# Kernel optimization log

Measured on AMD Instinct MI355X. Metric: run time of the kernel, lower is better.

The kernel has to match this reference:

```python
import jax, jax.numpy as jnp
import numpy as np

LOG2 = 0.6931471805599453

def ssp(x):
    # shifted softplus: softplus(x) - log(2)
    return jax.nn.softplus(x) - LOG2

def residual(v, W, b):
    # PhysNetResidual reuses the same linear twice: linear(act(linear(act(x)))) + x
    h = ssp(v) @ W + b
    h = ssp(h) @ W + b
    return h + v

def setup_inputs() -> dict:
    key = jax.random.key(0)
    ks = jax.random.split(key, 20)
    N, E, D, R = 50000, 600000, 128, 32
    n_int, n_atom_res, n_out_res = 3, 1, 1
    def orth(k, shape):
        return jax.random.orthogonal(k, shape[0])[: shape[0], : shape[1]].astype(jnp.float32) if shape[0] == shape[1] else jax.random.normal(k, shape, jnp.float32) * (1.0 / np.sqrt(shape[0]))
    return {
        "x": jax.random.normal(ks[0], (N, D), jnp.float32),
        "g_ij": jax.random.uniform(ks[1], (E, R), jnp.float32),
        "Wf": orth(ks[2], (D, D)), "bf": jnp.zeros((D,), jnp.float32),
        "Wg": jax.random.normal(ks[3], (R, D), jnp.float32) * (1.0 / np.sqrt(R)),
        "Wj": orth(ks[4], (D, D)), "bj": jnp.zeros((D,), jnp.float32),
        "Wi": orth(ks[5], (D, D)), "bi": jnp.zeros((D,), jnp.float32),
        "u": jnp.ones((D,), jnp.float32),
        "rWint": jnp.stack([orth(ks[6 + i], (D, D)) for i in range(n_int)]),
        "rbint": jnp.zeros((n_int, D), jnp.float32),
        "rWatom": jnp.stack([orth(ks[10 + i], (D, D)) for i in range(n_atom_res)]),
        "rbatom": jnp.zeros((n_atom_res, D), jnp.float32),
        "rWout": jnp.stack([orth(ks[12 + i], (D, D)) for i in range(n_out_res)]),
        "rbout": jnp.zeros((n_out_res, D), jnp.float32),
        "idx_i": jax.random.randint(ks[14], (E,), 0, N, jnp.int32),
        "idx_j": jax.random.randint(ks[15], (E,), 0, N, jnp.int32),
        "n_atoms": N,
    }

def reference(x, g_ij, Wf, bf, Wg, Wj, bj, Wi, bi, u,
              rWint, rbint, rWatom, rbatom, rWout, rbout,
              idx_i, idx_j, n_atoms):
    # --- PhysNetInteraction ---
    xa = ssp(x)                                   # [N, D]
    x_j = xa[idx_j]                               # gather -> [E, D]
    xp = u * xa                                   # [N, D]
    vp = ssp(x_j @ Wj + bj) * (g_ij @ Wg)         # [E, D] RBF-gated messages
    vm = ssp(xa @ Wi + bi)                        # [N, D]
    v = jax.ops.segment_sum(vp, idx_i, num_segments=n_atoms) + vm
    for k in range(rWint.shape[0]):
        v = residual(v, rWint[k], rbint[k])
    v = ssp(v)
    h = xp + v @ Wf + bf                          # [N, D]
    # --- atomic residual stack ---
    for k in range(rWatom.shape[0]):
        h = residual(h, rWatom[k], rbatom[k])
    # --- PhysNetOutput ---
    o = h
    for k in range(rWout.shape[0]):
        o = residual(o, rWout[k], rbout[k])
    o = ssp(o)
    return (o, h)
```

## Files before the change

### kernel.cpp

```cpp
#include <hip/hip_runtime.h>
#include <stdint.h>

#define LOG2F 0.693147180559945f

typedef __attribute__((ext_vector_type(8))) short short8;
typedef __attribute__((ext_vector_type(4))) float f32x4;

__device__ __forceinline__ float ssp(float x){
  float t = __expf(-fabsf(x));
  return fmaxf(x, 0.0f) + __logf(1.0f + t) - LOG2F;
}

__device__ __forceinline__ uint32_t bf16rn(float x){
  uint32_t u = __float_as_uint(x);
  return (u + 0x7fffu + ((u >> 16) & 1u)) >> 16;
}
__device__ __forceinline__ void split2(float x, unsigned short &h, unsigned short &l){
  uint32_t hb = bf16rn(x);
  h = (unsigned short)hb;
  float hf = __uint_as_float(hb << 16);
  l = (unsigned short)bf16rn(x - hf);
}


__global__ __launch_bounds__(256) void k_xconv(
    const float* __restrict__ x, unsigned short* __restrict__ xs, int total)
{
  int i = (blockIdx.x * 256 + threadIdx.x) * 4;
  if (i >= total) return;
  int row = i >> 7, col = i & 127;
  float4 f4 = *(const float4*)(x + i);
  ushort4 h4, l4;
  split2(ssp(f4.x), h4.x, l4.x);
  split2(ssp(f4.y), h4.y, l4.y);
  split2(ssp(f4.z), h4.z, l4.z);
  split2(ssp(f4.w), h4.w, l4.w);
  *(ushort4*)(xs + (size_t)row * 256 + col)       = h4;
  *(ushort4*)(xs + (size_t)row * 256 + 128 + col) = l4;
}

__global__ __launch_bounds__(256) void k_wconv(
    const float* __restrict__ Wj, const float* __restrict__ Wg,
    const float* __restrict__ Wi, const float* __restrict__ Wf,
    const float* __restrict__ Wint, const float* __restrict__ Watm,
    const float* __restrict__ Wout,
    unsigned short* __restrict__ ws, int ni, int na, int no)
{
  const int nmat = 3 + ni + na + no;
  int t = blockIdx.x * 256 + threadIdx.x;
  int m = t >> 11, r = t & 2047;
  if (m < nmat){
    const float* src;
    if      (m == 0)           src = Wj;
    else if (m == 1)           src = Wi;
    else if (m <= 1 + ni)      src = Wint + (size_t)(m - 2) * 16384;
    else if (m == 2 + ni)      src = Wf;
    else if (m <= 2 + ni + na) src = Watm + (size_t)(m - 3 - ni) * 16384;
    else                       src = Wout + (size_t)(m - 3 - ni - na) * 16384;
    int lane = r & 63, s = (r >> 6) & 3, ct = r >> 8;
    int col = ct * 16 + (lane & 15);
    int k0  = s * 32 + (lane >> 4) * 8;
    union { unsigned short u[8]; uint4 v; } H, L;
#pragma unroll
    for (int i = 0; i < 8; ++i) split2(src[(size_t)(k0 + i) * 128 + col], H.u[i], L.u[i]);
    ((uint4*)ws)[(size_t)m * 4096 + ((ct * 4 + s) * 2 + 0) * 64 + lane] = H.v;
    ((uint4*)ws)[(size_t)m * 4096 + ((ct * 4 + s) * 2 + 1) * 64 + lane] = L.v;
  } else {
    int uu = t - nmat * 2048;
    if (uu < 512){
      int lane = uu & 63, ct = uu >> 6;
      int col = ct * 16 + (lane & 15);
      int k0  = (lane >> 4) * 8;
      union { unsigned short u8[8]; uint4 v; } H, L;
#pragma unroll
      for (int i = 0; i < 8; ++i) split2(Wg[(size_t)(k0 + i) * 128 + col], H.u8[i], L.u8[i]);
      ((uint4*)ws)[(size_t)nmat * 4096 + (ct * 2 + 0) * 64 + lane] = H.v;
      ((uint4*)ws)[(size_t)nmat * 4096 + (ct * 2 + 1) * 64 + lane] = L.v;
    }
  }
}

__global__ __launch_bounds__(256) void k_edge(
    const unsigned short* __restrict__ xs, const float* __restrict__ g,
    const int* __restrict__ idx_i, const int* __restrict__ idx_j,
    const short8* __restrict__ wjf, const short8* __restrict__ wgf,
    const float* __restrict__ bj, float* vacc, int E)
{
  __shared__ short8 ahl[1024];
  __shared__ short8 ghl[256];
  __shared__ int    ii_s[32];

  const int t    = threadIdx.x;
  const int lane = t & 63;
  const int w    = t >> 6;
  const int l15  = lane & 15;
  const int lq   = lane >> 4;
  const int e0   = blockIdx.x * 32;

  {
    const int row = t >> 3, kseg = t & 7;
    int e = e0 + row; if (e >= E) e = E - 1;
    const int j = idx_j[e];
    const short8* xp = (const short8*)(xs + (size_t)j * 256);
    const int q0 = kseg * 2;
    short8 fh0 = xp[q0    ];
    short8 fh1 = xp[q0 + 1];
    short8 fl0 = xp[16 + q0    ];
    short8 fl1 = xp[16 + q0 + 1];
    ahl[0*512 + (q0+0)*32 + (row ^ (q0+0))] = fh0;
    ahl[0*512 + (q0+1)*32 + (row ^ (q0+1))] = fh1;
    ahl[1*512 + (q0+0)*32 + (row ^ (q0+0))] = fl0;
    ahl[1*512 + (q0+1)*32 + (row ^ (q0+1))] = fl1;
  }
  if (t < 64){
    const int row = t >> 1, kseg = t & 1;
    int e = e0 + row; if (e >= E) e = E - 1;
    const float4* gp = (const float4*)(g + (size_t)e * 32 + kseg * 16);
    short8 fh0, fh1, fl0, fl1;
#pragma unroll
    for (int q = 0; q < 4; ++q){
      float4 f4 = gp[q];
      float vv[4] = {f4.x, f4.y, f4.z, f4.w};
#pragma unroll
      for (int uu = 0; uu < 4; ++uu){
        unsigned short hh, ll;
        split2(vv[uu], hh, ll);
        int i = q * 4 + uu;
        if (i < 8){ fh0[i]   = (short)hh; fl0[i]   = (short)ll; }
        else      { fh1[i-8] = (short)hh; fl1[i-8] = (short)ll; }
      }
    }
    const int q0 = kseg * 2;
    ghl[0*128 + (q0+0)*32 + (row ^ (q0+0))] = fh0;
    ghl[0*128 + (q0+1)*32 + (row ^ (q0+1))] = fh1;
    ghl[1*128 + (q0+0)*32 + (row ^ (q0+0))] = fl0;
    ghl[1*128 + (q0+1)*32 + (row ^ (q0+1))] = fl1;
  }
  if (t >= 64 && t < 96){
    int rr = t - 64; int e = e0 + rr;
    ii_s[rr] = (e < E) ? idx_i[e] : -1;
  }
  __syncthreads();

  f32x4 am[2][2], ag[2][2];
#pragma unroll
  for (int a = 0; a < 2; ++a)
#pragma unroll
    for (int b = 0; b < 2; ++b){
      am[a][b] = (f32x4){0.f, 0.f, 0.f, 0.f};
      ag[a][b] = (f32x4){0.f, 0.f, 0.f, 0.f};
    }

#pragma unroll
  for (int s = 0; s < 4; ++s){
    const int q = s * 4 + lq;
    short8 a0h = ahl[0*512 + q*32 + ((l15     ) ^ q)];
    short8 a0l = ahl[1*512 + q*32 + ((l15     ) ^ q)];
    short8 a1h = ahl[0*512 + q*32 + ((16 + l15) ^ q)];
    short8 a1l = ahl[1*512 + q*32 + ((16 + l15) ^ q)];
#pragma unroll
    for (int c = 0; c < 2; ++c){
      const int ct = w * 2 + c;
      short8 bh = wjf[((ct*4 + s)*2 + 0)*64 + lane];
      short8 bl = wjf[((ct*4 + s)*2 + 1)*64 + lane];
      am[0][c] = __builtin_amdgcn_mfma_f32_16x16x32_bf16(a0h, bh, am[0][c], 0, 0, 0);
      am[0][c] = __builtin_amdgcn_mfma_f32_16x16x32_bf16(a0h, bl, am[0][c], 0, 0, 0);
      am[0][c] = __builtin_amdgcn_mfma_f32_16x16x32_bf16(a0l, bh, am[0][c], 0, 0, 0);
      am[1][c] = __builtin_amdgcn_mfma_f32_16x16x32_bf16(a1h, bh, am[1][c], 0, 0, 0);
      am[1][c] = __builtin_amdgcn_mfma_f32_16x16x32_bf16(a1h, bl, am[1][c], 0, 0, 0);
      am[1][c] = __builtin_amdgcn_mfma_f32_16x16x32_bf16(a1l, bh, am[1][c], 0, 0, 0);
    }
  }
  {
    const int q = lq;
    short8 g0h = ghl[0*128 + q*32 + ((l15     ) ^ q)];
    short8 g0l = ghl[1*128 + q*32 + ((l15     ) ^ q)];
    short8 g1h = ghl[0*128 + q*32 + ((16 + l15) ^ q)];
    short8 g1l = ghl[1*128 + q*32 + ((16 + l15) ^ q)];
#pragma unroll
    for (int c = 0; c < 2; ++c){
      const int ct = w * 2 + c;
      short8 bh = wgf[(ct*2 + 0)*64 + lane];
      short8 bl = wgf[(ct*2 + 1)*64 + lane];
      ag[0][c] = __builtin_amdgcn_mfma_f32_16x16x32_bf16(g0h, bh, ag[0][c], 0, 0, 0);
      ag[0][c] = __builtin_amdgcn_mfma_f32_16x16x32_bf16(g0h, bl, ag[0][c], 0, 0, 0);
      ag[0][c] = __builtin_amdgcn_mfma_f32_16x16x32_bf16(g0l, bh, ag[0][c], 0, 0, 0);
      ag[1][c] = __builtin_amdgcn_mfma_f32_16x16x32_bf16(g1h, bh, ag[1][c], 0, 0, 0);
      ag[1][c] = __builtin_amdgcn_mfma_f32_16x16x32_bf16(g1h, bl, ag[1][c], 0, 0, 0);
      ag[1][c] = __builtin_amdgcn_mfma_f32_16x16x32_bf16(g1l, bh, ag[1][c], 0, 0, 0);
    }
  }

#pragma unroll
  for (int c = 0; c < 2; ++c){
    const int col = (w * 2 + c) * 16 + l15;
    const float bjv = bj[col];
#pragma unroll
    for (int rt = 0; rt < 2; ++rt){
#pragma unroll
      for (int r = 0; r < 4; ++r){
        const int row = rt * 16 + lq * 4 + r;
        const int ii  = ii_s[row];
        if (ii >= 0){
          float vp = ssp(am[rt][c][r] + bjv) * ag[rt][c][r];
          atomicAdd(&vacc[(size_t)ii * 128 + col], vp);
        }
      }
    }
  }
}

__global__ __launch_bounds__(256) void k_chain(
    const float* __restrict__ x, const float* vacc,
    const short8* __restrict__ wcf,
    const float* __restrict__ bi, const float* __restrict__ bf_,
    const float* __restrict__ u,
    const float* __restrict__ bint, const float* __restrict__ batm,
    const float* __restrict__ bout,
    float* out, int N, int ni, int na, int no)
{
  __shared__ __align__(16) float arow[32][132];
  __shared__ short8 ahl[1024];

  const int t    = threadIdx.x;
  const int lane = t & 63;
  const int w    = t >> 6;
  const int l15  = lane & 15;
  const int lq   = lane >> 4;
  const int r0   = blockIdx.x * 32;
  const int srow = t >> 3, skseg = t & 7;

  const int col0 = (w*2 + 0)*16 + l15;
  const int col1 = (w*2 + 1)*16 + l15;

  f32x4 am[2][2];

  auto stage = [&](){
    const float* p = &arow[srow][skseg*16];
    short8 fh0, fh1, fl0, fl1;
#pragma unroll
    for (int i = 0; i < 8; ++i){
      unsigned short hh, ll;
      split2(p[i], hh, ll);
      fh0[i] = (short)hh; fl0[i] = (short)ll;
    }
#pragma unroll
    for (int i = 0; i < 8; ++i){
      unsigned short hh, ll;
      split2(p[8+i], hh, ll);
      fh1[i] = (short)hh; fl1[i] = (short)ll;
    }
    const int q0 = skseg * 2;
    ahl[0*512 + (q0+0)*32 + (srow ^ (q0+0))] = fh0;
    ahl[0*512 + (q0+1)*32 + (srow ^ (q0+1))] = fh1;
    ahl[1*512 + (q0+0)*32 + (srow ^ (q0+0))] = fl0;
    ahl[1*512 + (q0+1)*32 + (srow ^ (q0+1))] = fl1;
  };

  auto gemm = [&](const short8* __restrict__ wf){
#pragma unroll
    for (int a = 0; a < 2; ++a)
#pragma unroll
      for (int b = 0; b < 2; ++b) am[a][b] = (f32x4){0.f, 0.f, 0.f, 0.f};
#pragma unroll
    for (int s = 0; s < 4; ++s){
      const int q = s * 4 + lq;
      short8 a0h = ahl[0*512 + q*32 + ((l15     ) ^ q)];
      short8 a0l = ahl[1*512 + q*32 + ((l15     ) ^ q)];
      short8 a1h = ahl[0*512 + q*32 + ((16 + l15) ^ q)];
      short8 a1l = ahl[1*512 + q*32 + ((16 + l15) ^ q)];
#pragma unroll
      for (int c = 0; c < 2; ++c){
        const int ct = w * 2 + c;
        short8 bh = wf[((ct*4 + s)*2 + 0)*64 + lane];
        short8 bl = wf[((ct*4 + s)*2 + 1)*64 + lane];
        am[0][c] = __builtin_amdgcn_mfma_f32_16x16x32_bf16(a0h, bh, am[0][c], 0, 0, 0);
        am[0][c] = __builtin_amdgcn_mfma_f32_16x16x32_bf16(a0h, bl, am[0][c], 0, 0, 0);
        am[0][c] = __builtin_amdgcn_mfma_f32_16x16x32_bf16(a0l, bh, am[0][c], 0, 0, 0);
        am[1][c] = __builtin_amdgcn_mfma_f32_16x16x32_bf16(a1h, bh, am[1][c], 0, 0, 0);
        am[1][c] = __builtin_amdgcn_mfma_f32_16x16x32_bf16(a1h, bl, am[1][c], 0, 0, 0);
        am[1][c] = __builtin_amdgcn_mfma_f32_16x16x32_bf16(a1l, bh, am[1][c], 0, 0, 0);
      }
    }
  };

  auto put_ssp = [&](float (&st)[2][2][4]){
#pragma unroll
    for (int rt = 0; rt < 2; ++rt)
#pragma unroll
      for (int r = 0; r < 4; ++r){
        const int row = rt*16 + lq*4 + r;
        arow[row][col0] = ssp(st[rt][0][r]);
        arow[row][col1] = ssp(st[rt][1][r]);
      }
  };

  auto residual = [&](float (&st)[2][2][4], const short8* wf, const float* bvec){
    const float b0 = bvec[col0], b1 = bvec[col1];
    put_ssp(st);
    __syncthreads();
    stage();
    __syncthreads();
    gemm(wf);
#pragma unroll
    for (int rt = 0; rt < 2; ++rt)
#pragma unroll
      for (int r = 0; r < 4; ++r){
        const int row = rt*16 + lq*4 + r;
        arow[row][col0] = ssp(am[rt][0][r] + b0);
        arow[row][col1] = ssp(am[rt][1][r] + b1);
      }
    __syncthreads();
    stage();
    __syncthreads();
    gemm(wf);
#pragma unroll
    for (int rt = 0; rt < 2; ++rt)
#pragma unroll
      for (int r = 0; r < 4; ++r){
        st[rt][0][r] += am[rt][0][r] + b0;
        st[rt][1][r] += am[rt][1][r] + b1;
      }
  };

  {
    int row = r0 + srow; if (row >= N) row = N - 1;
    const float4* xp = (const float4*)(x + (size_t)row*128 + skseg*16);
    float* p = &arow[srow][skseg*16];
#pragma unroll
    for (int qq = 0; qq < 4; ++qq){
      float4 f4 = xp[qq];
      p[qq*4+0] = ssp(f4.x); p[qq*4+1] = ssp(f4.y);
      p[qq*4+2] = ssp(f4.z); p[qq*4+3] = ssp(f4.w);
    }
    stage();
  }
  __syncthreads();

  float xar[2][2][4];
#pragma unroll
  for (int rt = 0; rt < 2; ++rt)
#pragma unroll
    for (int r = 0; r < 4; ++r){
      const int row = rt*16 + lq*4 + r;
      xar[rt][0][r] = arow[row][col0];
      xar[rt][1][r] = arow[row][col1];
    }

  gemm(wcf + 0);
  float vst[2][2][4];
  {
    const float b0 = bi[col0], b1 = bi[col1];
#pragma unroll
    for (int rt = 0; rt < 2; ++rt)
#pragma unroll
      for (int r = 0; r < 4; ++r){
        int row = r0 + rt*16 + lq*4 + r; if (row >= N) row = N - 1;
        vst[rt][0][r] = vacc[(size_t)row*128 + col0] + ssp(am[rt][0][r] + b0);
        vst[rt][1][r] = vacc[(size_t)row*128 + col1] + ssp(am[rt][1][r] + b1);
      }
  }

  for (int kk = 0; kk < ni; ++kk)
    residual(vst, wcf + (size_t)(1 + kk) * 4096, bint + kk*128);

  put_ssp(vst);
  __syncthreads();
  stage();
  __syncthreads();
  gemm(wcf + (size_t)(1 + ni) * 4096);
  float hst[2][2][4];
  {
    const float b0 = bf_[col0], b1 = bf_[col1];
    const float u0 = u[col0],   u1 = u[col1];
#pragma unroll
    for (int rt = 0; rt < 2; ++rt)
#pragma unroll
      for (int r = 0; r < 4; ++r){
        hst[rt][0][r] = u0 * xar[rt][0][r] + am[rt][0][r] + b0;
        hst[rt][1][r] = u1 * xar[rt][1][r] + am[rt][1][r] + b1;
      }
  }

  for (int kk = 0; kk < na; ++kk)
    residual(hst, wcf + (size_t)(2 + ni + kk) * 4096, batm + kk*128);

#pragma unroll
  for (int rt = 0; rt < 2; ++rt)
#pragma unroll
    for (int r = 0; r < 4; ++r){
      const int row = r0 + rt*16 + lq*4 + r;
      if (row < N){
        out[(size_t)N*128 + (size_t)row*128 + col0] = hst[rt][0][r];
        out[(size_t)N*128 + (size_t)row*128 + col1] = hst[rt][1][r];
      }
    }

  for (int kk = 0; kk < no; ++kk)
    residual(hst, wcf + (size_t)(2 + ni + na + kk) * 4096, bout + kk*128);

#pragma unroll
  for (int rt = 0; rt < 2; ++rt)
#pragma unroll
    for (int r = 0; r < 4; ++r){
      const int row = r0 + rt*16 + lq*4 + r;
      if (row < N){
        out[(size_t)row*128 + col0] = ssp(hst[rt][0][r]);
        out[(size_t)row*128 + col1] = ssp(hst[rt][1][r]);
      }
    }
}

extern "C" void kernel_launch(void* const* d_in, const int* in_sizes, int n_in,
                              void* d_out, int out_size, void* d_ws, size_t ws_size,
                              hipStream_t stream)
{
  const float* x    = (const float*)d_in[0];
  const float* g    = (const float*)d_in[1];
  const float* Wf   = (const float*)d_in[2];
  const float* bf_  = (const float*)d_in[3];
  const float* Wg   = (const float*)d_in[4];
  const float* Wj   = (const float*)d_in[5];
  const float* bj   = (const float*)d_in[6];
  const float* Wi   = (const float*)d_in[7];
  const float* bi   = (const float*)d_in[8];
  const float* u    = (const float*)d_in[9];
  const float* Wint = (const float*)d_in[10];
  const float* bint = (const float*)d_in[11];
  const float* Watm = (const float*)d_in[12];
  const float* batm = (const float*)d_in[13];
  const float* Wout = (const float*)d_in[14];
  const float* bout = (const float*)d_in[15];
  const int* idx_i  = (const int*)d_in[16];
  const int* idx_j  = (const int*)d_in[17];

  const int N  = in_sizes[0] / 128;
  const int E  = in_sizes[16];
  const int ni = in_sizes[10] / 16384;
  const int na = in_sizes[12] / 16384;
  const int no = in_sizes[14] / 16384;

  const int nmat = 3 + ni + na + no;

  float* vacc = (float*)d_out;
  short8* wsf = (short8*)d_ws;
  const short8* wjf = wsf;
  const short8* wcf = wsf + (size_t)1 * 4096;
  const short8* wgf = wsf + (size_t)nmat * 4096;

  const size_t frag_bytes = (size_t)(nmat + 1) * 65536;
  const size_t xs_bytes   = (size_t)N * 256 * sizeof(unsigned short);
  unsigned short* xs;
  if (ws_size >= frag_bytes + xs_bytes)
    xs = (unsigned short*)((char*)d_ws + frag_bytes);
  else
    xs = (unsigned short*)((float*)d_out + (size_t)N * 128);

  hipMemsetAsync(vacc, 0, (size_t)N * 128 * sizeof(float), stream);
  k_xconv<<<dim3((N*128/4 + 255)/256), dim3(256), 0, stream>>>(x, xs, N * 128);
  k_wconv<<<dim3((nmat + 1) * 8), dim3(256), 0, stream>>>(Wj, Wg, Wi, Wf, Wint, Watm, Wout,
                                                          (unsigned short*)d_ws, ni, na, no);
  k_edge <<<dim3((E + 31)/32), dim3(256), 0, stream>>>(xs, g, idx_i, idx_j,
                                                       wjf, wgf, bj, vacc, E);
  k_chain<<<dim3((N + 31)/32), dim3(256), 0, stream>>>(x, vacc, wcf,
                                                       bi, bf_, u, bint, batm, bout,
                                                       (float*)d_out, N, ni, na, no);
}
```

Measured before the change: 589.5 us.

## Sort edges by destination and pre-reduce segment sums before atomics

Builds a counting-sort permutation of edges by idx_i (histogram, scan, scatter) and has the edge kernel process edges in sorted order. Each block stages its message tile in shared memory and merges consecutive rows with the same destination before issuing atomics. This targets the very large number of global float atomics in the segment sum. It adds several small preprocessing kernels and makes gathers of g indirect through the permutation.

```diff
diff --git a/kernel.cpp b/kernel.cpp
--- a/kernel.cpp
+++ b/kernel.cpp
@@ -37,6 +37,66 @@
   split2(ssp(f4.w), h4.w, l4.w);
   *(ushort4*)(xs + (size_t)row * 256 + col)       = h4;
   *(ushort4*)(xs + (size_t)row * 256 + 128 + col) = l4;
+}
+
+__global__ __launch_bounds__(256) void k_hist(
+    const int* __restrict__ idx_i, int* __restrict__ cnt, int E)
+{
+  int e = blockIdx.x * 256 + threadIdx.x;
+  if (e < E) atomicAdd(&cnt[idx_i[e]], 1);
+}
+
+__global__ __launch_bounds__(256) void k_scan1(
+    int* __restrict__ cnt, int* __restrict__ bsums, int N)
+{
+  __shared__ int sh[256];
+  const int t = threadIdx.x;
+  const int base = blockIdx.x * 2048 + t * 8;
+  int loc[8], s = 0;
+#pragma unroll
+  for (int k = 0; k < 8; ++k){
+    int v = (base + k < N) ? cnt[base + k] : 0;
+    loc[k] = s; s += v;
+  }
+  sh[t] = s;
+  __syncthreads();
+  const int own = s;
+  for (int off = 1; off < 256; off <<= 1){
+    int v = (t >= off) ? sh[t - off] : 0;
+    __syncthreads();
+    sh[t] += v;
+    __syncthreads();
+  }
+  const int ex = sh[t] - own;
+#pragma unroll
+  for (int k = 0; k < 8; ++k)
+    if (base + k < N) cnt[base + k] = ex + loc[k];
+  if (t == 255) bsums[blockIdx.x] = sh[255];
+}
+
+__global__ void k_scan2(int* __restrict__ bsums, int nblk){
+  if (threadIdx.x == 0 && blockIdx.x == 0){
+    int run = 0;
+    for (int b = 0; b < nblk; ++b){ int v = bsums[b]; bsums[b] = run; run += v; }
+  }
+}
+
+__global__ __launch_bounds__(256) void k_scan3(
+    int* __restrict__ cnt, const int* __restrict__ bsums, int N)
+{
+  int i = blockIdx.x * 256 + threadIdx.x;
+  if (i < N) cnt[i] += bsums[i >> 11];
+}
+
+__global__ __launch_bounds__(256) void k_scatter(
+    const int* __restrict__ idx_i, int* __restrict__ ofs,
+    int* __restrict__ perm, int E)
+{
+  int e = blockIdx.x * 256 + threadIdx.x;
+  if (e < E){
+    int p = atomicAdd(&ofs[idx_i[e]], 1);
+    perm[p] = e;
+  }
 }
 
 __global__ __launch_bounds__(256) void k_wconv(
@@ -83,12 +143,15 @@
 __global__ __launch_bounds__(256) void k_edge(
     const unsigned short* __restrict__ xs, const float* __restrict__ g,
     const int* __restrict__ idx_i, const int* __restrict__ idx_j,
+    const int* __restrict__ perm,
     const short8* __restrict__ wjf, const short8* __restrict__ wgf,
     const float* __restrict__ bj, float* vacc, int E)
 {
-  __shared__ short8 ahl[1024];
-  __shared__ short8 ghl[256];
-  __shared__ int    ii_s[32];
+  __shared__ __align__(16) char smem[16384 + 4096];
+  short8* ahl = (short8*)smem;
+  short8* ghl = (short8*)(smem + 16384);
+  float*  vp_s = (float*)smem;
+  __shared__ int ii_s[32];
 
   const int t    = threadIdx.x;
   const int lane = t & 63;
@@ -99,7 +162,8 @@
 
   {
     const int row = t >> 3, kseg = t & 7;
-    int e = e0 + row; if (e >= E) e = E - 1;
+    const int pe = e0 + row;
+    const int e = (pe < E) ? perm[pe] : 0;
     const int j = idx_j[e];
     const short8* xp = (const short8*)(xs + (size_t)j * 256);
     const int q0 = kseg * 2;
@@ -114,7 +178,8 @@
   }
   if (t < 64){
     const int row = t >> 1, kseg = t & 1;
-    int e = e0 + row; if (e >= E) e = E - 1;
+    const int pe = e0 + row;
+    const int e = (pe < E) ? perm[pe] : 0;
     const float4* gp = (const float4*)(g + (size_t)e * 32 + kseg * 16);
     short8 fh0, fh1, fl0, fl1;
 #pragma unroll
@@ -137,8 +202,8 @@
     ghl[1*128 + (q0+1)*32 + (row ^ (q0+1))] = fl1;
   }
   if (t >= 64 && t < 96){
-    int rr = t - 64; int e = e0 + rr;
-    ii_s[rr] = (e < E) ? idx_i[e] : -1;
+    int rr = t - 64, pe = e0 + rr;
+    ii_s[rr] = (pe < E) ? idx_i[perm[pe]] : -1;
   }
   __syncthreads();
 
@@ -191,22 +256,34 @@
     }
   }
 
+  __syncthreads();
 #pragma unroll
   for (int c = 0; c < 2; ++c){
     const int col = (w * 2 + c) * 16 + l15;
     const float bjv = bj[col];
 #pragma unroll
-    for (int rt = 0; rt < 2; ++rt){
+    for (int rt = 0; rt < 2; ++rt)
 #pragma unroll
       for (int r = 0; r < 4; ++r){
         const int row = rt * 16 + lq * 4 + r;
-        const int ii  = ii_s[row];
-        if (ii >= 0){
-          float vp = ssp(am[rt][c][r] + bjv) * ag[rt][c][r];
-          atomicAdd(&vacc[(size_t)ii * 128 + col], vp);
-        }
-      }
-    }
+        vp_s[row * 132 + col] = ssp(am[rt][c][r] + bjv) * ag[rt][c][r];
+      }
+  }
+  __syncthreads();
+  if (t < 128){
+    const int col = t;
+    float acc = vp_s[col];
+    int cur = ii_s[0];
+    for (int r = 1; r < 32; ++r){
+      const int ii = ii_s[r];
+      const float v = vp_s[r * 132 + col];
+      if (ii == cur) acc += v;
+      else {
+        if (cur >= 0) atomicAdd(&vacc[(size_t)cur * 128 + col], acc);
+        acc = v; cur = ii;
+      }
+    }
+    if (cur >= 0) atomicAdd(&vacc[(size_t)cur * 128 + col], acc);
   }
 }
 
@@ -449,20 +526,31 @@
   const short8* wgf = wsf + (size_t)nmat * 4096;
 
   const size_t frag_bytes = (size_t)(nmat + 1) * 65536;
-  const size_t xs_bytes   = (size_t)N * 256 * sizeof(unsigned short);
-  unsigned short* xs;
-  if (ws_size >= frag_bytes + xs_bytes)
-    xs = (unsigned short*)((char*)d_ws + frag_bytes);
-  else
-    xs = (unsigned short*)((float*)d_out + (size_t)N * 128);
+  int* cnt   = (int*)((char*)d_ws + frag_bytes);
+  int* bsums = cnt + N;
+  int* perm  = bsums + 1024;
+  char* after = (char*)(perm + E);
+  const size_t used = (size_t)(after - (char*)d_ws);
+  const size_t xs_bytes = (size_t)N * 256 * sizeof(unsigned short);
+  unsigned short* xs = (ws_size >= used + xs_bytes)
+      ? (unsigned short*)after
+      : (unsigned short*)((float*)d_out + (size_t)N * 128);
+
+  const int nblk = (N + 2047) / 2048;
 
   hipMemsetAsync(vacc, 0, (size_t)N * 128 * sizeof(float), stream);
-  k_xconv<<<dim3((N*128/4 + 255)/256), dim3(256), 0, stream>>>(x, xs, N * 128);
-  k_wconv<<<dim3((nmat + 1) * 8), dim3(256), 0, stream>>>(Wj, Wg, Wi, Wf, Wint, Watm, Wout,
-                                                          (unsigned short*)d_ws, ni, na, no);
-  k_edge <<<dim3((E + 31)/32), dim3(256), 0, stream>>>(xs, g, idx_i, idx_j,
-                                                       wjf, wgf, bj, vacc, E);
-  k_chain<<<dim3((N + 31)/32), dim3(256), 0, stream>>>(x, vacc, wcf,
-                                                       bi, bf_, u, bint, batm, bout,
-                                                       (float*)d_out, N, ni, na, no);
-}
+  hipMemsetAsync(cnt, 0, (size_t)N * sizeof(int), stream);
+  k_xconv  <<<dim3((N*128/4 + 255)/256), dim3(256), 0, stream>>>(x, xs, N * 128);
+  k_wconv  <<<dim3((nmat + 1) * 8), dim3(256), 0, stream>>>(Wj, Wg, Wi, Wf, Wint, Watm, Wout,
+                                                            (unsigned short*)d_ws, ni, na, no);
+  k_hist   <<<dim3((E + 255)/256), dim3(256), 0, stream>>>(idx_i, cnt, E);
+  k_scan1  <<<dim3(nblk), dim3(256), 0, stream>>>(cnt, bsums, N);
+  k_scan2  <<<dim3(1), dim3(64), 0, stream>>>(bsums, nblk);
+  k_scan3  <<<dim3((N + 255)/256), dim3(256), 0, stream>>>(cnt, bsums, N);
+  k_scatter<<<dim3((E + 255)/256), dim3(256), 0, stream>>>(idx_i, cnt, perm, E);
+  k_edge   <<<dim3((E + 31)/32), dim3(256), 0, stream>>>(xs, g, idx_i, idx_j, perm,
+                                                         wjf, wgf, bj, vacc, E);
+  k_chain  <<<dim3((N + 31)/32), dim3(256), 0, stream>>>(x, vacc, wcf,
+                                                         bi, bf_, u, bint, batm, bout,
+                                                         (float*)d_out, N, ni, na, no);
+}
```

New measurement: 535.7 us. 9.1% less time.
